# Optimization experiments

Hardware: AMD Instinct MI355X
Metric: run time of the kernel (lower is better)

The kernel has to match this reference:

```python
import jax, jax.numpy as jnp
import numpy as np
from jax import lax

BS = 8  # block size
NF = 64  # num_feat

def _dct_mat(n=BS):
    k = np.arange(n)
    D = np.cos(np.pi * (2 * k[None, :] + 1) * k[:, None] / (2 * n)) * np.sqrt(2.0 / n)
    D[0] = np.sqrt(1.0 / n)
    return jnp.asarray(D, dtype=jnp.float32)  # orthonormal DCT-II basis [8,8]

D_DCT = _dct_mat()

def conv2d(x, w, b, stride=1, padding=0, dilation=1, groups=1):
    out = lax.conv_general_dilated(
        x, w, window_strides=(stride, stride),
        padding=[(padding, padding), (padding, padding)],
        rhs_dilation=(dilation, dilation),
        feature_group_count=groups,
        dimension_numbers=('NCHW', 'OIHW', 'NCHW'))
    return out + b[None, :, None, None]

def block_dct_idct(x, bs=BS):
    # fused per-8x8-block DDCT followed by IDDCT (orthonormal basis ->
    # mathematically identity, computed explicitly as in the original loop)
    B, C, H, W = x.shape
    xb = x.reshape(B, C, H // bs, bs, W // bs, bs)
    CB = jnp.einsum('ij,bchjwk,lk->bchiwl', D_DCT, xb, D_DCT)   # D X D^T
    out = jnp.einsum('ji,bchjwk,kl->bchiwl', D_DCT, CB, D_DCT)  # D^T Y D
    return out.reshape(B, C, H, W)

def setup_inputs() -> dict:
    key = jax.random.key(0)
    ks = jax.random.split(key, 16)
    s = 0.05
    inp = {
        'x': jax.random.normal(ks[0], (2, 72, 256, 256), dtype=jnp.float32),
        'conv_w': jax.random.normal(ks[1], (64, 72, 3, 3), dtype=jnp.float32) * s,
        'conv_b': jnp.zeros((64,), dtype=jnp.float32),
        # 7 distinct directional_dct_layer instances (branch 6 reuses layer 4's weights, as in the source)
        'ddct_w': jax.random.normal(ks[2], (7, 64, 64, 3, 3), dtype=jnp.float32) * s,
        'ddct_b': jnp.zeros((7, 64), dtype=jnp.float32),
        'dctc_w': jax.random.normal(ks[3], (7, 64, 1, 3, 3), dtype=jnp.float32) * s,  # groups=64 depthwise
        'dctc_b': jnp.zeros((7, 64), dtype=jnp.float32),
        'dw1_w': jax.random.normal(ks[4], (32, 72, 3, 3), dtype=jnp.float32) * s,
        'dw1_b': jnp.zeros((32,), dtype=jnp.float32),
        'dw3_w': jax.random.normal(ks[5], (512, 32, 1, 1), dtype=jnp.float32) * s,
        'dw3_b': jnp.zeros((512,), dtype=jnp.float32),
        'ar_w': jax.random.normal(ks[6], (72, 512, 3, 3), dtype=jnp.float32) * s,
        'ar_b': jnp.zeros((72,), dtype=jnp.float32),
    }
    return inp

def reference(x, conv_w, conv_b, ddct_w, ddct_b, dctc_w, dctc_b,
              dw1_w, dw1_b, dw3_w, dw3_b, ar_w, ar_b):
    B, _, H, W = x.shape
    feat = jax.nn.gelu(conv2d(x, conv_w, conv_b, padding=1), approximate=False)
    # branches use layers [0,1,3,4,5,6(->4),7,8]; branch 6 reuses conv_dct_4
    layer_idx = [0, 1, 2, 3, 4, 3, 5, 6]
    outs = []
    for li in layer_idx:
        y = jax.nn.gelu(conv2d(feat, ddct_w[li], ddct_b[li], padding=1), approximate=False) + feat
        y = conv2d(y, dctc_w[li], dctc_b[li], stride=8, padding=2, dilation=2, groups=NF)
        y = block_dct_idct(y)
        y = jax.image.resize(y, (B, NF, H, W), method='bilinear')  # align_corners=False
        outs.append(y)
    w = jax.nn.sigmoid(conv2d(jax.nn.relu(conv2d(x, dw1_w, dw1_b, padding=1)), dw3_w, dw3_b, padding=0))
    gated = jnp.concatenate([o * w[:, i * NF:(i + 1) * NF] for i, o in enumerate(outs)], axis=1)
    return conv2d(gated, ar_w, ar_b, padding=1)
```

## Files before the change

kernel.cpp:

```cpp
#include <hip/hip_runtime.h>
#include <hip/hip_bf16.h>

#define BB 2
#define HH 256
#define WW 256
#define HW (HH*WW)
#define GP 258
#define GPP (GP*GP)

typedef __attribute__((ext_vector_type(8))) short bf16x8;
typedef __attribute__((ext_vector_type(4))) float f32x4;

__device__ __forceinline__ float geluf(float x) {
    return 0.5f * x * (1.0f + erff(x * 0.7071067811865475f));
}

__device__ __forceinline__ ushort f2bf(float f) {
    __hip_bfloat16 h = __float2bfloat16(f);
    return *reinterpret_cast<ushort*>(&h);
}
__device__ __forceinline__ float bf2f(ushort u) {
    uint v = ((uint)u) << 16;
    return *reinterpret_cast<float*>(&v);
}

__device__ __forceinline__ int dec96(int i) {
    int q = i / 3, r = i - q * 3;
    return q * 8 + (r == 0 ? 0 : (r == 1 ? 2 : 6));
}

__global__ __launch_bounds__(256) void xpose_kernel(
    const float* __restrict__ x, ushort* __restrict__ xt)
{
    const int pix = blockIdx.x * 256 + threadIdx.x;
    const int b   = pix >> 16;
    const int rem = pix & 65535;

    uint w[48];
    const float* xb = x + (size_t)b * 72 * HW + rem;
    #pragma unroll
    for (int i = 0; i < 36; ++i) {
        const ushort lo = f2bf(xb[(size_t)(2 * i)     * HW]);
        const ushort hi = f2bf(xb[(size_t)(2 * i + 1) * HW]);
        w[i] = (uint)lo | ((uint)hi << 16);
    }
    #pragma unroll
    for (int i = 36; i < 48; ++i) w[i] = 0;

    uint* dst = reinterpret_cast<uint*>(xt + (size_t)pix * 96);
    #pragma unroll
    for (int k = 0; k < 12; ++k) {
        uint4 u = { w[4*k], w[4*k+1], w[4*k+2], w[4*k+3] };
        *reinterpret_cast<uint4*>(dst + 4 * k) = u;
    }
}

__global__ __launch_bounds__(256) void prepack_w1_kernel(
    const float* __restrict__ conv_w, const float* __restrict__ dw1_w,
    ushort* __restrict__ wpc1)
{
    const int idx = blockIdx.x * 256 + threadIdx.x;
    if (idx >= 9 * 3 * 6 * 64) return;
    const int lane = idx & 63;
    int rest = idx >> 6;
    const int mf = rest % 6; rest /= 6;
    const int cb = rest % 3;
    const int t  = rest / 3;
    const int co  = mf * 16 + (lane & 15);
    const int ci0 = cb * 32 + (lane >> 4) * 8;
    ushort* dst = wpc1 + (size_t)idx * 8;
    #pragma unroll
    for (int j = 0; j < 8; ++j) {
        const int ci = ci0 + j;
        float w = 0.0f;
        if (ci < 72)
            w = (co < 64) ? conv_w[((size_t)co * 72 + ci) * 9 + t]
                          : dw1_w[((size_t)(co - 64) * 72 + ci) * 9 + t];
        dst[j] = f2bf(w);
    }
}

__global__ __launch_bounds__(256) void conv1dw1_mfma_kernel(
    const ushort* __restrict__ xt, const ushort* __restrict__ wpc1,
    const float* __restrict__ conv_b, const float* __restrict__ dw1_b,
    ushort* __restrict__ fg, float* __restrict__ relu1)
{
    const int lane = threadIdx.x & 63;
    const int wave = threadIdx.x >> 6;
    const int l15  = lane & 15;
    const int lg   = lane >> 4;

    const int bid  = blockIdx.x;
    const int b    = bid >> 9;
    const int rest = bid & 511;
    const int y    = rest >> 1;
    const int x0   = (rest & 1) * 128 + wave * 32;

    f32x4 acc[6][2];
    #pragma unroll
    for (int mf = 0; mf < 6; ++mf)
        #pragma unroll
        for (int nf = 0; nf < 2; ++nf)
            acc[mf][nf] = (f32x4){0.f, 0.f, 0.f, 0.f};

    const bf16x8 zero8 = {};

    #pragma unroll 1
    for (int t = 0; t < 9; ++t) {
        const int dy = t / 3 - 1, dx = t % 3 - 1;
        const int yy = y + dy;
        if ((unsigned)yy >= (unsigned)HH) continue;

        const int xA = x0 + l15 + dx;
        const int xB = xA + 16;
        const bool va = (unsigned)xA < (unsigned)WW;
        const bool vb = (unsigned)xB < (unsigned)WW;
        const int xAc = min(max(xA, 0), WW - 1);
        const int xBc = min(xB, WW - 1);

        const ushort* rowbase = xt + ((size_t)(b * HH + yy) * WW) * 96;
        const ushort* pA = rowbase + (size_t)xAc * 96 + lg * 8;
        const ushort* pB = rowbase + (size_t)xBc * 96 + lg * 8;
        const ushort* wp = wpc1 + (size_t)(t * 3) * (6 * 512) + lane * 8;

        #pragma unroll
        for (int cb = 0; cb < 3; ++cb) {
            bf16x8 B0 = *reinterpret_cast<const bf16x8*>(pA + cb * 32);
            bf16x8 B1 = *reinterpret_cast<const bf16x8*>(pB + cb * 32);
            B0 = va ? B0 : zero8;
            B1 = vb ? B1 : zero8;
            const ushort* wpc = wp + (size_t)cb * (6 * 512);
            #pragma unroll
            for (int mf = 0; mf < 6; ++mf) {
                const bf16x8 A = *reinterpret_cast<const bf16x8*>(wpc + mf * 512);
                acc[mf][0] = __builtin_amdgcn_mfma_f32_16x16x32_bf16(A, B0, acc[mf][0], 0, 0, 0);
                acc[mf][1] = __builtin_amdgcn_mfma_f32_16x16x32_bf16(A, B1, acc[mf][1], 0, 0, 0);
            }
        }
    }

    #pragma unroll
    for (int nf = 0; nf < 2; ++nf) {
        const int xx = x0 + nf * 16 + l15;
        ushort* fgp = fg + ((size_t)(b * HH + y) * WW + xx) * 64;
        #pragma unroll
        for (int mf = 0; mf < 4; ++mf) {
            const int co = mf * 16 + lg * 4;
            ushort pk[4];
            #pragma unroll
            for (int r = 0; r < 4; ++r)
                pk[r] = f2bf(geluf(acc[mf][nf][r] + conv_b[co + r]));
            *reinterpret_cast<uint2*>(fgp + co) = *reinterpret_cast<uint2*>(pk);
        }
    }
    #pragma unroll
    for (int mf = 4; mf < 6; ++mf) {
        const int co = (mf - 4) * 16 + lg * 4;
        #pragma unroll
        for (int nf = 0; nf < 2; ++nf) {
            const int xx = x0 + nf * 16 + l15;
            float* op = relu1 + ((size_t)(b * 32 + co) * HH + y) * WW + xx;
            #pragma unroll
            for (int r = 0; r < 4; ++r)
                op[(size_t)r * HW] = fmaxf(acc[mf][nf][r] + dw1_b[co + r], 0.0f);
        }
    }
}

__global__ __launch_bounds__(256) void prepack_wb_kernel(
    const float* __restrict__ ddct_w, ushort* __restrict__ wpb)
{
    const int idx = blockIdx.x * 256 + threadIdx.x;
    if (idx >= 7 * 9 * 2 * 4 * 64) return;
    const int lane = idx & 63;
    int rest = idx >> 6;
    const int mf = rest & 3; rest >>= 2;
    const int cb = rest & 1; rest >>= 1;
    const int t  = rest % 9;
    const int li = rest / 9;
    const int co  = mf * 16 + (lane & 15);
    const int ci0 = cb * 32 + (lane >> 4) * 8;
    ushort* dst = wpb + (size_t)idx * 8;
    #pragma unroll
    for (int j = 0; j < 8; ++j)
        dst[j] = f2bf(ddct_w[(((size_t)li * 64 + co) * 64 + ci0 + j) * 9 + t]);
}

__global__ __launch_bounds__(256) void branch_mfma_kernel(
    const ushort* __restrict__ fg, const ushort* __restrict__ wpb,
    const float* __restrict__ ddct_b, float* __restrict__ ycomp)
{
    const int lane = threadIdx.x & 63;
    const int wave = threadIdx.x >> 6;
    const int l15  = lane & 15;
    const int lg   = lane >> 4;

    int bid = blockIdx.x;
    const int t72 = bid % 72; bid /= 72;
    const int b  = bid & 1;
    const int li = bid >> 1;
    const int widx = t72 * 4 + wave;
    const int r  = widx / 3;
    const int c0 = (widx - r * 3) * 32;
    const int R  = dec96(r);

    const int cA = c0 + l15, cB = cA + 16;
    const int CA = dec96(cA), CB2 = dec96(cB);

    f32x4 acc[4][2];
    #pragma unroll
    for (int mf = 0; mf < 4; ++mf)
        #pragma unroll
        for (int nf = 0; nf < 2; ++nf)
            acc[mf][nf] = (f32x4){0.f, 0.f, 0.f, 0.f};

    const bf16x8 zero8 = {};
    const ushort* fgb = fg + (size_t)b * HW * 64;

    #pragma unroll 1
    for (int t = 0; t < 9; ++t) {
        const int dy = t / 3 - 1, dx = t % 3 - 1;
        const int yy = R + dy;
        if ((unsigned)yy >= (unsigned)HH) continue;

        const int xA = CA + dx, xB = CB2 + dx;
        const bool va = (unsigned)xA < (unsigned)WW;
        const bool vb = (unsigned)xB < (unsigned)WW;
        const int xAc = min(max(xA, 0), WW - 1);
        const int xBc = min(max(xB, 0), WW - 1);

        const ushort* rowb = fgb + (size_t)yy * WW * 64;
        const ushort* pA = rowb + (size_t)xAc * 64 + lg * 8;
        const ushort* pB = rowb + (size_t)xBc * 64 + lg * 8;
        const ushort* wp = wpb + (size_t)((li * 9 + t) * 2) * (4 * 512) + lane * 8;

        #pragma unroll
        for (int cb = 0; cb < 2; ++cb) {
            bf16x8 B0 = *reinterpret_cast<const bf16x8*>(pA + cb * 32);
            bf16x8 B1 = *reinterpret_cast<const bf16x8*>(pB + cb * 32);
            B0 = va ? B0 : zero8;
            B1 = vb ? B1 : zero8;
            const ushort* wpc = wp + (size_t)cb * (4 * 512);
            #pragma unroll
            for (int mf = 0; mf < 4; ++mf) {
                const bf16x8 A = *reinterpret_cast<const bf16x8*>(wpc + mf * 512);
                acc[mf][0] = __builtin_amdgcn_mfma_f32_16x16x32_bf16(A, B0, acc[mf][0], 0, 0, 0);
                acc[mf][1] = __builtin_amdgcn_mfma_f32_16x16x32_bf16(A, B1, acc[mf][1], 0, 0, 0);
            }
        }
    }

    #pragma unroll
    for (int nf = 0; nf < 2; ++nf) {
        const int c = c0 + nf * 16 + l15;
        const int C = dec96(c);
        const ushort* res = fgb + ((size_t)R * WW + C) * 64;
        #pragma unroll
        for (int mf = 0; mf < 4; ++mf) {
            const int co = mf * 16 + lg * 4;
            ushort r4[4];
            *reinterpret_cast<uint2*>(r4) = *reinterpret_cast<const uint2*>(res + co);
            #pragma unroll
            for (int rr = 0; rr < 4; ++rr) {
                const float v = geluf(acc[mf][nf][rr] + ddct_b[li * 64 + co + rr]) + bf2f(r4[rr]);
                ycomp[((((size_t)li * BB + b) * 64 + co + rr) * 96 + r) * 96 + c] = v;
            }
        }
    }
}

__global__ __launch_bounds__(256) void dctc_kernel(
    const float* __restrict__ ycomp, const float* __restrict__ dctc_w,
    const float* __restrict__ dctc_b, float* __restrict__ s_all)
{
    const int idx = blockIdx.x * 256 + threadIdx.x;
    if (idx >= 7 * BB * 64 * 32 * 32) return;
    const int ow = idx & 31;
    const int oh = (idx >> 5) & 31;
    const int c  = (idx >> 10) & 63;
    const int b  = (idx >> 16) & (BB - 1);
    const int li = idx >> 17;

    const float* yc = ycomp + (((size_t)li * BB + b) * 64 + c) * (96 * 96);
    const float* w  = dctc_w + (li * 64 + c) * 9;
    float acc = dctc_b[li * 64 + c];
    #pragma unroll
    for (int ky = 0; ky < 3; ++ky) {
        const int cr = 3 * oh + ky - 1;
        if (cr < 0) continue;
        #pragma unroll
        for (int kx = 0; kx < 3; ++kx) {
            const int cc = 3 * ow + kx - 1;
            if (cc < 0) continue;
            acc = fmaf(yc[cr * 96 + cc], w[ky * 3 + kx], acc);
        }
    }
    s_all[idx] = acc;
}

__global__ __launch_bounds__(256) void prepack_w3_kernel(
    const float* __restrict__ dw3_w, float* __restrict__ dw3t)
{
    const int idx = blockIdx.x * 256 + threadIdx.x;
    if (idx >= 32 * 512) return;
    const int ch = idx & 511;
    const int k  = idx >> 9;
    dw3t[k * 512 + ch] = dw3_w[ch * 32 + k];
}

__global__ __launch_bounds__(256) void halo_zero_kernel(ushort* __restrict__ gt)
{
    const int PB = 2 * GP * 64 + 2 * 256 * 64;
    const int i = blockIdx.x * 256 + threadIdx.x;
    if (i >= BB * PB) return;
    const int b = i / PB;
    int r = i - b * PB;
    size_t px;
    int c4;
    if (r < 2 * GP * 64) {
        const int rr = r / (GP * 64);
        int rem = r - rr * (GP * 64);
        const int xp = rem / 64; c4 = rem % 64;
        px = (size_t)(rr ? GP - 1 : 0) * GP + xp;
    } else {
        r -= 2 * GP * 64;
        const int side = r / (256 * 64);
        int rem = r - side * (256 * 64);
        const int yp = 1 + rem / 64; c4 = rem % 64;
        px = (size_t)yp * GP + (side ? GP - 1 : 0);
    }
    const uint4 z = {0u, 0u, 0u, 0u};
    *reinterpret_cast<uint4*>(gt + ((size_t)b * GPP + px) * 512 + c4 * 8) = z;
}

__global__ __launch_bounds__(256, 3) void gated_nhwc_kernel(
    const float* __restrict__ relu1, const float* __restrict__ dw3t,
    const float* __restrict__ dw3_b, const float* __restrict__ s_all,
    ushort* __restrict__ gt)
{
    __shared__ float sm[32][32];
    const int pix0 = blockIdx.x * 32;
    const int b  = pix0 >> 16;
    const int y  = (pix0 >> 8) & 255;
    const int x0 = pix0 & 255;

    {
        const int spx = threadIdx.x & 31;
        const int k0  = threadIdx.x >> 5;
        const float* rbase = relu1 + (size_t)b * 32 * HW + (size_t)y * WW + x0 + spx;
        #pragma unroll
        for (int i = 0; i < 4; ++i)
            sm[k0 + 8 * i][spx] = rbase[(size_t)(k0 + 8 * i) * HW];
    }
    __syncthreads();

    const int ch0 = threadIdx.x * 2;
    const int branch = ch0 >> 6;
    const int c0 = ch0 & 63;
    const int lmap[8] = {0, 1, 2, 3, 4, 3, 5, 6};
    const int li = lmap[branch];

    const float bb0 = dw3_b[ch0], bb1 = dw3_b[ch0 + 1];

    float2 wreg[32];
    #pragma unroll
    for (int k = 0; k < 32; ++k)
        wreg[k] = *reinterpret_cast<const float2*>(dw3t + k * 512 + ch0);

    float acc0[32], acc1[32];
    #pragma unroll
    for (int px = 0; px < 32; ++px) { acc0[px] = bb0; acc1[px] = bb1; }

    #pragma unroll
    for (int k = 0; k < 32; ++k) {
        const float w0k = wreg[k].x;
        const float w1k = wreg[k].y;
        const float4* row = reinterpret_cast<const float4*>(&sm[k][0]);
        #pragma unroll
        for (int q = 0; q < 8; ++q) {
            const float4 r4 = row[q];
            acc0[q*4+0] = fmaf(r4.x, w0k, acc0[q*4+0]);
            acc0[q*4+1] = fmaf(r4.y, w0k, acc0[q*4+1]);
            acc0[q*4+2] = fmaf(r4.z, w0k, acc0[q*4+2]);
            acc0[q*4+3] = fmaf(r4.w, w0k, acc0[q*4+3]);
            acc1[q*4+0] = fmaf(r4.x, w1k, acc1[q*4+0]);
            acc1[q*4+1] = fmaf(r4.y, w1k, acc1[q*4+1]);
            acc1[q*4+2] = fmaf(r4.z, w1k, acc1[q*4+2]);
            acc1[q*4+3] = fmaf(r4.w, w1k, acc1[q*4+3]);
        }
    }

    const float* sp0 = s_all + (((size_t)li * BB + b) * 64 + c0) * 1024;
    const float* sp1 = sp0 + 1024;

    const float sy = (y + 0.5f) * 0.125f - 0.5f;
    const float fy0f = floorf(sy);
    const float fy = sy - fy0f;
    int y0 = (int)fy0f;
    const int y1 = min(y0 + 1, 31);
    y0 = max(y0, 0);

    float n0[6], n1[6];
    const int xb = (x0 >> 3) - 1;
    #pragma unroll
    for (int jj = 0; jj < 6; ++jj) {
        const int xn = min(max(xb + jj, 0), 31);
        const float a00 = sp0[y0 * 32 + xn], a01 = sp0[y1 * 32 + xn];
        const float a10 = sp1[y0 * 32 + xn], a11 = sp1[y1 * 32 + xn];
        n0[jj] = a00 + fy * (a01 - a00);
        n1[jj] = a10 + fy * (a11 - a10);
    }

    ushort* gbase = gt + (((size_t)b * GPP) + (size_t)(y + 1) * GP + (x0 + 1)) * 512 + ch0;
    #pragma unroll
    for (int px = 0; px < 32; ++px) {
        const int   j  = (px + 4) >> 3;
        const float fx = (float)((px + 4) & 7) * 0.125f + 0.0625f;
        const float va = n0[j] + fx * (n0[j + 1] - n0[j]);
        const float vb = n1[j] + fx * (n1[j + 1] - n1[j]);
        const float g0 = 1.0f / (1.0f + exp2f(-1.4426950408889634f * acc0[px]));
        const float g1 = 1.0f / (1.0f + exp2f(-1.4426950408889634f * acc1[px]));
        const uint pack = (uint)f2bf(va * g0) | ((uint)f2bf(vb * g1) << 16);
        *reinterpret_cast<uint*>(gbase + (size_t)px * 512) = pack;
    }
}

__global__ __launch_bounds__(256) void prepack_w_kernel(
    const float* __restrict__ ar_w, ushort* __restrict__ wpA,
    ushort* __restrict__ wpB)
{
    const int idx = blockIdx.x * 256 + threadIdx.x;
    if (idx >= 9 * 16 * 5 * 64) return;
    const int lane = idx & 63;
    int rest = idx >> 6;
    const int mf = rest % 5; rest /= 5;
    const int cb = rest % 16;
    const int t  = rest / 16;
    const int co  = mf * 16 + (lane & 15);
    const int ci0 = cb * 32 + (lane >> 4) * 8;
    ushort* dst = (mf < 4)
        ? wpA + ((((size_t)(t * 16 + cb) * 4 + mf) * 64 + lane) * 8)
        : wpB + (((size_t)(t * 16 + cb) * 64 + lane) * 8);
    #pragma unroll
    for (int j = 0; j < 8; ++j) {
        const float w = (co < 72) ? ar_w[((size_t)co * 512 + ci0 + j) * 9 + t] : 0.0f;
        dst[j] = f2bf(w);
    }
}

#define WPA_TAP (16 * 4 * 512)

__global__ __launch_bounds__(256, 2) void conv_ar_mfma_kernel(
    const ushort* __restrict__ gt, const ushort* __restrict__ wpA,
    const ushort* __restrict__ wpB, const float* __restrict__ ar_b,
    float* __restrict__ out)
{
    __shared__ ushort smw[WPA_TAP];
    const int tid  = threadIdx.x;
    const int lane = tid & 63;
    const int wave = tid >> 6;
    const int l15  = lane & 15;
    const int lg   = lane >> 4;

    const int lb = (blockIdx.x & 7) * 64 + (blockIdx.x >> 3);
    const int b  = lb >> 8;
    const int y  = lb & 255;
    const int x0 = wave * 64;

    f32x4 acc[5][4];
    #pragma unroll
    for (int mf = 0; mf < 5; ++mf)
        #pragma unroll
        for (int nf = 0; nf < 4; ++nf)
            acc[mf][nf] = (f32x4){0.f, 0.f, 0.f, 0.f};

    #pragma unroll 1
    for (int t = 0; t < 9; ++t) {
        const int dy = t / 3, dx = t % 3;

        __syncthreads();
        {
            const uint4* src = reinterpret_cast<const uint4*>(wpA + (size_t)t * WPA_TAP);
            uint4* dst = reinterpret_cast<uint4*>(smw);
            #pragma unroll
            for (int i = 0; i < 16; ++i)
                dst[i * 256 + tid] = src[i * 256 + tid];
        }
        __syncthreads();

        const ushort* rowP = gt + ((size_t)b * GPP + (size_t)(y + dy) * GP) * 512;
        int off[4];
        #pragma unroll
        for (int nf = 0; nf < 4; ++nf)
            off[nf] = (x0 + nf * 16 + l15 + dx) * 512 + lg * 8;
        const ushort* wB_t = wpB + (size_t)t * (16 * 512) + lane * 8;

        #pragma unroll 4
        for (int cb = 0; cb < 16; ++cb) {
            bf16x8 Bv[4];
            #pragma unroll
            for (int nf = 0; nf < 4; ++nf)
                Bv[nf] = *reinterpret_cast<const bf16x8*>(rowP + off[nf] + cb * 32);
            const bf16x8 A4 = *reinterpret_cast<const bf16x8*>(wB_t + (size_t)cb * 512);
            #pragma unroll
            for (int mf = 0; mf < 4; ++mf) {
                const bf16x8 A = *reinterpret_cast<const bf16x8*>(smw + (cb * 4 + mf) * 512 + lane * 8);
                #pragma unroll
                for (int nf = 0; nf < 4; ++nf)
                    acc[mf][nf] = __builtin_amdgcn_mfma_f32_16x16x32_bf16(A, Bv[nf], acc[mf][nf], 0, 0, 0);
            }
            #pragma unroll
            for (int nf = 0; nf < 4; ++nf)
                acc[4][nf] = __builtin_amdgcn_mfma_f32_16x16x32_bf16(A4, Bv[nf], acc[4][nf], 0, 0, 0);
        }
    }

    #pragma unroll
    for (int mf = 0; mf < 5; ++mf) {
        const int co = mf * 16 + lg * 4;
        if (co >= 72) continue;
        #pragma unroll
        for (int nf = 0; nf < 4; ++nf) {
            const int x = x0 + nf * 16 + l15;
            float* op = out + (((size_t)(b * 72 + co) * HH + y) * WW) + x;
            #pragma unroll
            for (int r = 0; r < 4; ++r)
                op[(size_t)r * HW] = acc[mf][nf][r] + ar_b[co + r];
        }
    }
}

extern "C" void kernel_launch(void* const* d_in, const int* in_sizes, int n_in,
                              void* d_out, int out_size, void* d_ws, size_t ws_size,
                              hipStream_t stream) {
    const float* x      = (const float*)d_in[0];
    const float* conv_w = (const float*)d_in[1];
    const float* conv_b = (const float*)d_in[2];
    const float* ddct_w = (const float*)d_in[3];
    const float* ddct_b = (const float*)d_in[4];
    const float* dctc_w = (const float*)d_in[5];
    const float* dctc_b = (const float*)d_in[6];
    const float* dw1_w  = (const float*)d_in[7];
    const float* dw1_b  = (const float*)d_in[8];
    const float* dw3_w  = (const float*)d_in[9];
    const float* dw3_b  = (const float*)d_in[10];
    const float* ar_w   = (const float*)d_in[11];
    const float* ar_b   = (const float*)d_in[12];
    float* out = (float*)d_out;

    float* ws = (float*)d_ws;
    ushort* gated_t = (ushort*)ws;
    ushort* fg    = (ushort*)ws;
    float* ycomp  = ws + 4194304;
    float* s_all  = ws + 34080768;
    float* relu1  = ws + 34998272;
    ushort* wpA   = (ushort*)(ws + 39192576);
    ushort* wpB   = (ushort*)(ws + 39340032);
    ushort* wpb   = (ushort*)(ws + 39376896);
    ushort* wpc1  = (ushort*)(ws + 39505920);
    ushort* xt    = (ushort*)(ws + 39547392);
    float* dw3t   = ws + 45838848;

    prepack_w_kernel<<<dim3(180), dim3(256), 0, stream>>>(ar_w, wpA, wpB);
    prepack_wb_kernel<<<dim3(126), dim3(256), 0, stream>>>(ddct_w, wpb);
    prepack_w1_kernel<<<dim3(41), dim3(256), 0, stream>>>(conv_w, dw1_w, wpc1);
    prepack_w3_kernel<<<dim3(64), dim3(256), 0, stream>>>(dw3_w, dw3t);
    xpose_kernel<<<dim3(BB * HW / 256), dim3(256), 0, stream>>>(x, xt);

    conv1dw1_mfma_kernel<<<dim3(BB * HH * 2), dim3(256), 0, stream>>>(
        xt, wpc1, conv_b, dw1_b, fg, relu1);

    branch_mfma_kernel<<<dim3(7 * BB * 72), dim3(256), 0, stream>>>(
        fg, wpb, ddct_b, ycomp);

    dctc_kernel<<<dim3((7 * BB * 64 * 32 * 32) / 256), dim3(256), 0, stream>>>(
        ycomp, dctc_w, dctc_b, s_all);

    halo_zero_kernel<<<dim3(514), dim3(256), 0, stream>>>(gated_t);

    gated_nhwc_kernel<<<dim3(BB * HW / 32), dim3(256), 0, stream>>>(
        relu1, dw3t, dw3_b, s_all, gated_t);

    conv_ar_mfma_kernel<<<dim3(BB * HH), dim3(256), 0, stream>>>(
        gated_t, wpA, wpB, ar_b, out);
}
```

Measured before the change: 423.2 us.

## Split final conv reduction across two channel halves with bf16 partials and reduce kernel

The final 512->72 3x3 conv now splits input channels into two halves, doubling the grid to 1024 blocks. The loop order is swapped so the outer loop runs over channel blocks and the inner loop over the nine taps, with all five M-fragments read from a single repacked LDS weight chunk. Partial sums are written as bf16 to a workspace and summed with the bias by a new reduce kernel. The aim is more parallelism and occupancy (launch bounds 3), at the cost of an extra pass over memory and bf16 rounding of the partial sums before accumulation.

```diff
diff --git a/kernel.cpp b/kernel.cpp
--- a/kernel.cpp
+++ b/kernel.cpp
@@ -426,21 +426,18 @@
 }
 
 __global__ __launch_bounds__(256) void prepack_w_kernel(
-    const float* __restrict__ ar_w, ushort* __restrict__ wpA,
-    ushort* __restrict__ wpB)
+    const float* __restrict__ ar_w, ushort* __restrict__ wpack)
 {
     const int idx = blockIdx.x * 256 + threadIdx.x;
-    if (idx >= 9 * 16 * 5 * 64) return;
+    if (idx >= 16 * 9 * 5 * 64) return;
     const int lane = idx & 63;
     int rest = idx >> 6;
     const int mf = rest % 5; rest /= 5;
-    const int cb = rest % 16;
-    const int t  = rest / 16;
+    const int t  = rest % 9;
+    const int cb = rest / 9;
     const int co  = mf * 16 + (lane & 15);
     const int ci0 = cb * 32 + (lane >> 4) * 8;
-    ushort* dst = (mf < 4)
-        ? wpA + ((((size_t)(t * 16 + cb) * 4 + mf) * 64 + lane) * 8)
-        : wpB + (((size_t)(t * 16 + cb) * 64 + lane) * 8);
+    ushort* dst = wpack + (size_t)idx * 8;
     #pragma unroll
     for (int j = 0; j < 8; ++j) {
         const float w = (co < 72) ? ar_w[((size_t)co * 512 + ci0 + j) * 9 + t] : 0.0f;
@@ -448,23 +445,23 @@
     }
 }
 
-#define WPA_TAP (16 * 4 * 512)
-
-__global__ __launch_bounds__(256, 2) void conv_ar_mfma_kernel(
-    const ushort* __restrict__ gt, const ushort* __restrict__ wpA,
-    const ushort* __restrict__ wpB, const float* __restrict__ ar_b,
-    float* __restrict__ out)
-{
-    __shared__ ushort smw[WPA_TAP];
+#define WPK_CHUNK (9 * 5 * 512)
+
+__global__ __launch_bounds__(256, 3) void conv_ar_mfma_kernel(
+    const ushort* __restrict__ gt, const ushort* __restrict__ wpack,
+    ushort* __restrict__ part)
+{
+    __shared__ ushort smw[WPK_CHUNK];
     const int tid  = threadIdx.x;
     const int lane = tid & 63;
     const int wave = tid >> 6;
     const int l15  = lane & 15;
     const int lg   = lane >> 4;
 
-    const int lb = (blockIdx.x & 7) * 64 + (blockIdx.x >> 3);
-    const int b  = lb >> 8;
-    const int y  = lb & 255;
+    const int lb = (blockIdx.x & 7) * 128 + (blockIdx.x >> 3);
+    const int kh = lb & 1;
+    const int y  = (lb >> 1) & 255;
+    const int b  = lb >> 9;
     const int x0 = wave * 64;
 
     f32x4 acc[5][4];
@@ -474,47 +471,52 @@
         for (int nf = 0; nf < 4; ++nf)
             acc[mf][nf] = (f32x4){0.f, 0.f, 0.f, 0.f};
 
+    const ushort* rowp[3];
+    #pragma unroll
+    for (int dy = 0; dy < 3; ++dy)
+        rowp[dy] = gt + ((size_t)b * GPP + (size_t)(y + dy) * GP) * 512;
+    int off[3][4];
+    #pragma unroll
+    for (int dx = 0; dx < 3; ++dx)
+        #pragma unroll
+        for (int nf = 0; nf < 4; ++nf)
+            off[dx][nf] = (x0 + nf * 16 + l15 + dx) * 512 + lg * 8;
+
+    const int cb0 = kh * 8;
     #pragma unroll 1
-    for (int t = 0; t < 9; ++t) {
-        const int dy = t / 3, dx = t % 3;
-
+    for (int cbi = 0; cbi < 8; ++cbi) {
+        const int cb = cb0 + cbi;
         __syncthreads();
         {
-            const uint4* src = reinterpret_cast<const uint4*>(wpA + (size_t)t * WPA_TAP);
+            const uint4* src = reinterpret_cast<const uint4*>(wpack + (size_t)cb * WPK_CHUNK);
             uint4* dst = reinterpret_cast<uint4*>(smw);
             #pragma unroll
-            for (int i = 0; i < 16; ++i)
-                dst[i * 256 + tid] = src[i * 256 + tid];
+            for (int i = 0; i < 12; ++i) {
+                const int e = i * 256 + tid;
+                if (e < 2880) dst[e] = src[e];
+            }
         }
         __syncthreads();
 
-        const ushort* rowP = gt + ((size_t)b * GPP + (size_t)(y + dy) * GP) * 512;
-        int off[4];
-        #pragma unroll
-        for (int nf = 0; nf < 4; ++nf)
-            off[nf] = (x0 + nf * 16 + l15 + dx) * 512 + lg * 8;
-        const ushort* wB_t = wpB + (size_t)t * (16 * 512) + lane * 8;
-
-        #pragma unroll 4
-        for (int cb = 0; cb < 16; ++cb) {
+        const int cbo = cb * 32;
+        #pragma unroll
+        for (int t = 0; t < 9; ++t) {
+            const int dy = t / 3, dx = t % 3;
             bf16x8 Bv[4];
             #pragma unroll
             for (int nf = 0; nf < 4; ++nf)
-                Bv[nf] = *reinterpret_cast<const bf16x8*>(rowP + off[nf] + cb * 32);
-            const bf16x8 A4 = *reinterpret_cast<const bf16x8*>(wB_t + (size_t)cb * 512);
-            #pragma unroll
-            for (int mf = 0; mf < 4; ++mf) {
-                const bf16x8 A = *reinterpret_cast<const bf16x8*>(smw + (cb * 4 + mf) * 512 + lane * 8);
+                Bv[nf] = *reinterpret_cast<const bf16x8*>(rowp[dy] + off[dx][nf] + cbo);
+            #pragma unroll
+            for (int mf = 0; mf < 5; ++mf) {
+                const bf16x8 A = *reinterpret_cast<const bf16x8*>(smw + (t * 5 + mf) * 512 + lane * 8);
                 #pragma unroll
                 for (int nf = 0; nf < 4; ++nf)
                     acc[mf][nf] = __builtin_amdgcn_mfma_f32_16x16x32_bf16(A, Bv[nf], acc[mf][nf], 0, 0, 0);
             }
-            #pragma unroll
-            for (int nf = 0; nf < 4; ++nf)
-                acc[4][nf] = __builtin_amdgcn_mfma_f32_16x16x32_bf16(A4, Bv[nf], acc[4][nf], 0, 0, 0);
-        }
-    }
-
+        }
+    }
+
+    ushort* pb = part + (size_t)kh * ((size_t)BB * 72 * HW);
     #pragma unroll
     for (int mf = 0; mf < 5; ++mf) {
         const int co = mf * 16 + lg * 4;
@@ -522,12 +524,30 @@
         #pragma unroll
         for (int nf = 0; nf < 4; ++nf) {
             const int x = x0 + nf * 16 + l15;
-            float* op = out + (((size_t)(b * 72 + co) * HH + y) * WW) + x;
+            ushort* op = pb + (((size_t)(b * 72 + co) * HH + y) * WW) + x;
             #pragma unroll
             for (int r = 0; r < 4; ++r)
-                op[(size_t)r * HW] = acc[mf][nf][r] + ar_b[co + r];
-        }
-    }
+                op[(size_t)r * HW] = f2bf(acc[mf][nf][r]);
+        }
+    }
+}
+
+__global__ __launch_bounds__(256) void reduce_kernel(
+    const ushort* __restrict__ part, const float* __restrict__ ar_b,
+    float* __restrict__ out)
+{
+    const size_t base = ((size_t)blockIdx.x * 256 + threadIdx.x) * 4;
+    if (base >= (size_t)BB * 72 * HW) return;
+    const int ch = (int)((base >> 16) % 72);
+    const float bias = ar_b[ch];
+    const uint2 p0 = *reinterpret_cast<const uint2*>(part + base);
+    const uint2 p1 = *reinterpret_cast<const uint2*>(part + (size_t)BB * 72 * HW + base);
+    float4 o;
+    o.x = bf2f((ushort)(p0.x      )) + bf2f((ushort)(p1.x      )) + bias;
+    o.y = bf2f((ushort)(p0.x >> 16)) + bf2f((ushort)(p1.x >> 16)) + bias;
+    o.z = bf2f((ushort)(p0.y      )) + bf2f((ushort)(p1.y      )) + bias;
+    o.w = bf2f((ushort)(p0.y >> 16)) + bf2f((ushort)(p1.y >> 16)) + bias;
+    *reinterpret_cast<float4*>(out + base) = o;
 }
 
 extern "C" void kernel_launch(void* const* d_in, const int* in_sizes, int n_in,
@@ -554,14 +574,14 @@
     float* ycomp  = ws + 4194304;
     float* s_all  = ws + 34080768;
     float* relu1  = ws + 34998272;
-    ushort* wpA   = (ushort*)(ws + 39192576);
-    ushort* wpB   = (ushort*)(ws + 39340032);
-    ushort* wpb   = (ushort*)(ws + 39376896);
-    ushort* wpc1  = (ushort*)(ws + 39505920);
-    ushort* xt    = (ushort*)(ws + 39547392);
+    ushort* xt    = (ushort*)(ws + 39192576);
+    ushort* part  = (ushort*)(ws + 34998272);
+    ushort* wpack = (ushort*)(ws + 45484032);
+    ushort* wpb   = (ushort*)(ws + 45668352);
+    ushort* wpc1  = (ushort*)(ws + 45797376);
     float* dw3t   = ws + 45838848;
 
-    prepack_w_kernel<<<dim3(180), dim3(256), 0, stream>>>(ar_w, wpA, wpB);
+    prepack_w_kernel<<<dim3(180), dim3(256), 0, stream>>>(ar_w, wpack);
     prepack_wb_kernel<<<dim3(126), dim3(256), 0, stream>>>(ddct_w, wpb);
     prepack_w1_kernel<<<dim3(41), dim3(256), 0, stream>>>(conv_w, dw1_w, wpc1);
     prepack_w3_kernel<<<dim3(64), dim3(256), 0, stream>>>(dw3_w, dw3t);
@@ -581,6 +601,9 @@
     gated_nhwc_kernel<<<dim3(BB * HW / 32), dim3(256), 0, stream>>>(
         relu1, dw3t, dw3_b, s_all, gated_t);
 
-    conv_ar_mfma_kernel<<<dim3(BB * HH), dim3(256), 0, stream>>>(
-        gated_t, wpA, wpB, ar_b, out);
-}
+    conv_ar_mfma_kernel<<<dim3(BB * HH * 2), dim3(256), 0, stream>>>(
+        gated_t, wpack, part);
+
+    reduce_kernel<<<dim3((BB * 72 * HW / 4 + 255) / 256), dim3(256), 0, stream>>>(
+        part, ar_b, out);
+}
```

Result: slower. 442.0 us (+4.4%).
